# Kernel optimization log

Hardware: AMD Instinct MI355X
Metric: run time of the kernel (lower is better)

## Reference

```python
import jax, jax.numpy as jnp
import numpy as np

B, S, D, H = 256, 200, 256, 4
HD = D // H
R = 16  # HIE reduced rank (hardcoded in module)
EPS = 1e-12


def setup_inputs() -> dict:
    key = jax.random.key(0)
    ks = jax.random.split(key, 32)
    w = lambda k, sh: jax.random.normal(k, sh, jnp.float32) * 0.02
    inp = {
        'input_tensor': jax.random.normal(ks[0], (B, S, D), jnp.float32),
        'fusion_tensor': jax.random.normal(ks[1], (B, S, D), jnp.float32),
        'pos_tensor': jax.random.normal(ks[2], (B, S, D), jnp.float32),
        'attention_mask': jnp.zeros((B, 1, 1, S), jnp.float32),
        # projections (stored as (in, out); apply as x @ W + b)
        'Wv': w(ks[3], (D, D)), 'bv': w(ks[4], (D,)),
        'Wqf': w(ks[5], (D, D)), 'bqf': w(ks[6], (D,)),
        'Wkf': w(ks[7], (D, D)), 'bkf': w(ks[8], (D,)),
        'Wvf': w(ks[9], (D, D)), 'bvf': w(ks[10], (D,)),
        'Wqp': w(ks[11], (D, D)), 'bqp': w(ks[12], (D,)),
        'Wkp': w(ks[13], (D, D)), 'bkp': w(ks[14], (D,)),
        'Wvp': w(ks[15], (D, D)), 'bvp': w(ks[16], (D,)),
        # output dense + LayerNorm per branch
        'Wd': w(ks[17], (D, D)), 'bd': w(ks[18], (D,)),
        'g1': jnp.ones((D,), jnp.float32), 'b1': jnp.zeros((D,), jnp.float32),
        'Wfd': w(ks[19], (D, D)), 'bfd': w(ks[20], (D,)),
        'g2': jnp.ones((D,), jnp.float32), 'b2': jnp.zeros((D,), jnp.float32),
        'Wpd': w(ks[21], (D, D)), 'bpd': w(ks[22], (D,)),
        'g3': jnp.ones((D,), jnp.float32), 'b3': jnp.zeros((D,), jnp.float32),
        # HIE parameter (n, r)
        'Wr': jax.random.normal(ks[23], (S, R), jnp.float32),
    }
    return inp


def _heads(t):
    # (B,S,D) -> (B,H,S,HD)
    return t.reshape(B, S, H, HD).transpose(0, 2, 1, 3)


def _layernorm(x, g, b):
    m = jnp.mean(x, axis=-1, keepdims=True)
    v = jnp.mean((x - m) ** 2, axis=-1, keepdims=True)
    return (x - m) * jax.lax.rsqrt(v + EPS) * g + b


def _compute(resid, value_layer, scores, mask, Wd, bd, g, b):
    s = scores / np.sqrt(HD) + mask
    probs = jax.nn.softmax(s, axis=-1)  # (attn dropout = identity in eval)
    ctx = jnp.einsum('bhqk,bhkd->bhqd', probs, value_layer)
    ctx = ctx.transpose(0, 2, 1, 3).reshape(B, S, D)
    return _layernorm(ctx @ Wd + bd + resid, g, b)


def _hie(hX, hA, Wr):
    # reduce sequence dim, batched QR on (d, r) columns
    hr = jnp.einsum('bnd,nr->brd', hX, Wr)        # (B,R,D)
    Q, _ = jnp.linalg.qr(hr.transpose(0, 2, 1))   # (B,D,R), reduced
    pX = hX @ Q                                    # (B,S,R)
    pA = hA @ Q
    pAt = (pX * pA > 0).astype(pA.dtype) * pA      # indicator gate
    return jnp.einsum('bnr,bdr->bnd', pAt, Q)


def reference(input_tensor, fusion_tensor, pos_tensor, attention_mask,
              Wv, bv, Wqf, bqf, Wkf, bkf, Wvf, bvf, Wqp, bqp, Wkp, bkp,
              Wvp, bvp, Wd, bd, g1, b1, Wfd, bfd, g2, b2, Wpd, bpd, g3, b3, Wr):
    item_v = _heads(input_tensor @ Wv + bv)
    fq = _heads(fusion_tensor @ Wqf + bqf)
    fk = _heads(fusion_tensor @ Wkf + bkf)
    fv = _heads(fusion_tensor @ Wvf + bvf)
    pq = _heads(pos_tensor @ Wqp + bqp)
    pk = _heads(pos_tensor @ Wkp + bkp)
    pv = _heads(pos_tensor @ Wvp + bvp)

    item_scores = jnp.einsum('bhqd,bhkd->bhqk', fq, fk)
    pos_scores = jnp.einsum('bhqd,bhkd->bhqk', pq, pk)
    both_scores = item_scores + pos_scores

    h = _compute(input_tensor, item_v, both_scores, attention_mask, Wd, bd, g1, b1)
    hf = _compute(fusion_tensor, fv, item_scores, attention_mask, Wfd, bfd, g2, b2)
    hp = _compute(pos_tensor, pv, pos_scores, attention_mask, Wpd, bpd, g3, b3)

    h = h + _hie(h, hf, Wr)
    return (h, hf, hp)
```

## Files before the change

### kernel.cpp

```cpp
#include <hip/hip_runtime.h>


constexpr int B_ = 256, S_ = 200, D_ = 256, H_ = 4, R_ = 16;
constexpr int M_ = B_ * S_;
constexpr size_t BSD = (size_t)B_ * S_ * D_;

typedef __attribute__((ext_vector_type(8))) short bf16x8;
typedef __attribute__((ext_vector_type(4))) short bf16x4;
typedef __attribute__((ext_vector_type(4))) float f32x4;

#if __has_builtin(__builtin_amdgcn_mfma_f32_16x16x16bf16_1k)
#define MFMA16(A, B, C) __builtin_amdgcn_mfma_f32_16x16x16bf16_1k((A), (B), (C), 0, 0, 0)
#define HAVE_MFMA16 1
#else
#define HAVE_MFMA16 0
#endif

__device__ __forceinline__ float bf2f(unsigned short u) {
  union { unsigned int i; float f; } v; v.i = ((unsigned int)u) << 16; return v.f;
}
__device__ __forceinline__ unsigned short f2bf_rne(float f) {
  union { float f; unsigned int i; } v; v.f = f;
  unsigned int u = v.i;
  u += 0x7FFFu + ((u >> 16) & 1u);
  return (unsigned short)(u >> 16);
}
__device__ __forceinline__ void split4(const float* v, ushort4& hi, ushort4& lo) {
  unsigned short h0 = f2bf_rne(v[0]), h1 = f2bf_rne(v[1]);
  unsigned short h2 = f2bf_rne(v[2]), h3 = f2bf_rne(v[3]);
  hi.x = h0; hi.y = h1; hi.z = h2; hi.w = h3;
  lo.x = f2bf_rne(v[0] - bf2f(h0)); lo.y = f2bf_rne(v[1] - bf2f(h1));
  lo.z = f2bf_rne(v[2] - bf2f(h2)); lo.w = f2bf_rne(v[3] - bf2f(h3));
}
__device__ __forceinline__ void split8(const float* v, bf16x8& hi, bf16x8& lo) {
#pragma unroll
  for (int i = 0; i < 8; ++i) {
    unsigned short h = f2bf_rne(v[i]);
    hi[i] = (short)h;
    lo[i] = (short)f2bf_rne(v[i] - bf2f(h));
  }
}

struct GemmArgs {
  const float* X[7]; const float* bias[7]; float* Y[7];
  const float* resid[7]; const float* g[7]; const float* bvec[7];
  const unsigned short* stash;
};
struct WSplitArgs { const float* W[7]; };

__global__ __launch_bounds__(256) void split_w(WSplitArgs wa, unsigned short* stash)
{
  const int z = blockIdx.y;
  const int idx = blockIdx.x * 256 + threadIdx.x;
  const int k = idx >> 8, n = idx & 255;
  const float x = wa.W[z][idx];
  const unsigned short h = f2bf_rne(x);
  const unsigned short l = f2bf_rne(x - bf2f(h));
  const size_t o = (size_t)z * 131072 + (size_t)n * 256 + k;
  stash[o] = h;
  stash[o + 65536] = l;
}

template<bool LN>
__global__ __launch_bounds__(256, 2) void gemm_mfma(GemmArgs ga)
{
  __shared__ unsigned short lds[30720];
  unsigned short* Ah = lds;
  unsigned short* Al = Ah + 128 * 40;
  unsigned short* Bh = Al + 128 * 40;
  unsigned short* Bl = Bh + 256 * 40;
  const int t = threadIdx.x;
  const int z = blockIdx.y;
  const int m0 = blockIdx.x * 128;
  const float* __restrict__ X = ga.X[z];
  const float* __restrict__ bias = ga.bias[z];
  float* __restrict__ Y = ga.Y[z];
  const unsigned short* __restrict__ Wst = ga.stash + (size_t)z * 131072;
  const int w = t >> 6, lane = t & 63;
  const int wm = w >> 1, wn = w & 1;
  const int lrow = lane & 15;
  const int lk = (lane >> 4) << 3;
  const int rsub = (lane >> 4) << 2;

  f32x4 acc[4][8];
#pragma unroll
  for (int mf = 0; mf < 4; ++mf)
#pragma unroll
    for (int nf = 0; nf < 8; ++nf)
#pragma unroll
      for (int r = 0; r < 4; ++r) acc[mf][nf][r] = 0.f;

  for (int k0 = 0; k0 < 256; k0 += 32) {
#pragma unroll
    for (int i = 0; i < 2; ++i) {
      int c = t + i * 256;
      int r = c >> 2, c8 = (c & 3) << 3;
      float xv[8];
      *reinterpret_cast<float4*>(&xv[0]) =
          *reinterpret_cast<const float4*>(X + (size_t)(m0 + r) * 256 + k0 + c8);
      *reinterpret_cast<float4*>(&xv[4]) =
          *reinterpret_cast<const float4*>(X + (size_t)(m0 + r) * 256 + k0 + c8 + 4);
      bf16x8 hv, lv;
      split8(xv, hv, lv);
      *reinterpret_cast<bf16x8*>(&Ah[r * 40 + c8]) = hv;
      *reinterpret_cast<bf16x8*>(&Al[r * 40 + c8]) = lv;
    }
#pragma unroll
    for (int i = 0; i < 4; ++i) {
      int c = t + i * 256;
      int n = c >> 2, kc = (c & 3) << 3;
      *reinterpret_cast<uint4*>(&Bh[n * 40 + kc]) =
          *reinterpret_cast<const uint4*>(Wst + (size_t)n * 256 + k0 + kc);
      *reinterpret_cast<uint4*>(&Bl[n * 40 + kc]) =
          *reinterpret_cast<const uint4*>(Wst + 65536 + (size_t)n * 256 + k0 + kc);
    }
    __syncthreads();
    bf16x8 ah[4], al[4];
#pragma unroll
    for (int mf = 0; mf < 4; ++mf) {
      int r = wm * 64 + mf * 16 + lrow;
      ah[mf] = *reinterpret_cast<const bf16x8*>(&Ah[r * 40 + lk]);
      al[mf] = *reinterpret_cast<const bf16x8*>(&Al[r * 40 + lk]);
    }
#pragma unroll
    for (int nf = 0; nf < 8; ++nf) {
      int n = wn * 128 + nf * 16 + lrow;
      bf16x8 bh = *reinterpret_cast<const bf16x8*>(&Bh[n * 40 + lk]);
      bf16x8 bl = *reinterpret_cast<const bf16x8*>(&Bl[n * 40 + lk]);
#pragma unroll
      for (int mf = 0; mf < 4; ++mf) {
        acc[mf][nf] = __builtin_amdgcn_mfma_f32_16x16x32_bf16(ah[mf], bh, acc[mf][nf], 0, 0, 0);
        acc[mf][nf] = __builtin_amdgcn_mfma_f32_16x16x32_bf16(al[mf], bh, acc[mf][nf], 0, 0, 0);
        acc[mf][nf] = __builtin_amdgcn_mfma_f32_16x16x32_bf16(ah[mf], bl, acc[mf][nf], 0, 0, 0);
      }
    }
    __syncthreads();
  }

  if (!LN) {
#pragma unroll
    for (int nf = 0; nf < 8; ++nf) {
      const int coln = wn * 128 + nf * 16 + lrow;
      const float bb = bias[coln];
#pragma unroll
      for (int mf = 0; mf < 4; ++mf)
#pragma unroll
        for (int r = 0; r < 4; ++r) {
          const size_t row = (size_t)(m0 + wm * 64 + mf * 16 + rsub + r);
          Y[row * 256 + coln] = acc[mf][nf][r] + bb;
        }
    }
  } else {
    const float* __restrict__ resid = ga.resid[z];
    const float* __restrict__ gv = ga.g[z];
    const float* __restrict__ bv = ga.bvec[z];
    float s_[4][4], q_[4][4];
#pragma unroll
    for (int mf = 0; mf < 4; ++mf)
#pragma unroll
      for (int r = 0; r < 4; ++r) { s_[mf][r] = 0.f; q_[mf][r] = 0.f; }
#pragma unroll
    for (int nf = 0; nf < 8; ++nf) {
      const int coln = wn * 128 + nf * 16 + lrow;
      const float bb = bias[coln];
#pragma unroll
      for (int mf = 0; mf < 4; ++mf)
#pragma unroll
        for (int r = 0; r < 4; ++r) {
          const size_t row = (size_t)(m0 + wm * 64 + mf * 16 + rsub + r);
          float v = acc[mf][nf][r] + bb + resid[row * 256 + coln];
          acc[mf][nf][r] = v;
          s_[mf][r] += v;
          q_[mf][r] = fmaf(v, v, q_[mf][r]);
        }
    }
#pragma unroll
    for (int mf = 0; mf < 4; ++mf)
#pragma unroll
      for (int r = 0; r < 4; ++r) {
        float sv = s_[mf][r], qv = q_[mf][r];
        sv += __shfl_xor(sv, 1); qv += __shfl_xor(qv, 1);
        sv += __shfl_xor(sv, 2); qv += __shfl_xor(qv, 2);
        sv += __shfl_xor(sv, 4); qv += __shfl_xor(qv, 4);
        sv += __shfl_xor(sv, 8); qv += __shfl_xor(qv, 8);
        s_[mf][r] = sv; q_[mf][r] = qv;
      }
    __syncthreads();
    float* red = (float*)lds;
    if (lrow == 0) {
#pragma unroll
      for (int mf = 0; mf < 4; ++mf)
#pragma unroll
        for (int r = 0; r < 4; ++r) {
          int rl = wm * 64 + mf * 16 + rsub + r;
          red[rl * 4 + wn * 2 + 0] = s_[mf][r];
          red[rl * 4 + wn * 2 + 1] = q_[mf][r];
        }
    }
    __syncthreads();
#pragma unroll
    for (int mf = 0; mf < 4; ++mf)
#pragma unroll
      for (int r = 0; r < 4; ++r) {
        int rl = wm * 64 + mf * 16 + rsub + r;
        float st = red[rl * 4 + 0] + red[rl * 4 + 2];
        float qt = red[rl * 4 + 1] + red[rl * 4 + 3];
        float mean = st * (1.0f / 256.0f);
        float var = qt * (1.0f / 256.0f) - mean * mean;
        s_[mf][r] = mean;
        q_[mf][r] = rsqrtf(var + 1e-12f);
      }
#pragma unroll
    for (int nf = 0; nf < 8; ++nf) {
      const int coln = wn * 128 + nf * 16 + lrow;
      const float gg = gv[coln], be = bv[coln];
#pragma unroll
      for (int mf = 0; mf < 4; ++mf)
#pragma unroll
        for (int r = 0; r < 4; ++r) {
          const size_t row = (size_t)(m0 + wm * 64 + mf * 16 + rsub + r);
          Y[row * 256 + coln] = (acc[mf][nf][r] - s_[mf][r]) * q_[mf][r] * gg + be;
        }
    }
  }
}

__global__ __launch_bounds__(256) void attn_mfma(
    const float* __restrict__ Qf, const float* __restrict__ Kf,
    const float* __restrict__ Qp, const float* __restrict__ Kp,
    const float* __restrict__ Vi, const float* __restrict__ Vf,
    const float* __restrict__ Vp, const float* __restrict__ mask,
    float* __restrict__ Ch, float* __restrict__ Cf, float* __restrict__ Cp)
{
  __shared__ unsigned short su[21504];
  __shared__ float mt[32];
  constexpr int KFH = 0,     KFL = 2816,  KPH = 5632,  KPL = 8448;
  constexpr int VIH = 11264, VIL = 13824, VFH = 16384, VPH = 18944;
  const int t = threadIdx.x;
  const int mtile = blockIdx.x, h = blockIdx.y, b = blockIdx.z;
  const int w = t >> 6, lane = t & 63, lg = lane >> 4, lm = lane & 15;
  const int mbase = mtile * 128 + w * 32;
  const bool wactive = (mbase < 200);
  const size_t bh = (size_t)b * 200 * 256 + (size_t)h * 64;

  bf16x8 qfh[2][2], qfl[2][2], qph[2][2], qpl[2][2];
#pragma unroll
  for (int mf2 = 0; mf2 < 2; ++mf2) {
    int gq = mbase + mf2 * 16 + lm; if (gq > 199) gq = 199;
    const size_t qb = bh + (size_t)gq * 256;
#pragma unroll
    for (int ks = 0; ks < 2; ++ks) {
      float qv[8];
      *reinterpret_cast<float4*>(&qv[0]) =
          *reinterpret_cast<const float4*>(Qf + qb + ks * 32 + lg * 8);
      *reinterpret_cast<float4*>(&qv[4]) =
          *reinterpret_cast<const float4*>(Qf + qb + ks * 32 + lg * 8 + 4);
      split8(qv, qfh[mf2][ks], qfl[mf2][ks]);
      *reinterpret_cast<float4*>(&qv[0]) =
          *reinterpret_cast<const float4*>(Qp + qb + ks * 32 + lg * 8);
      *reinterpret_cast<float4*>(&qv[4]) =
          *reinterpret_cast<const float4*>(Qp + qb + ks * 32 + lg * 8 + 4);
      split8(qv, qph[mf2][ks], qpl[mf2][ks]);
    }
  }

  f32x4 aH[4][2], aF[4][2], aP[4][2];
#pragma unroll
  for (int df = 0; df < 4; ++df)
#pragma unroll
    for (int mf2 = 0; mf2 < 2; ++mf2)
#pragma unroll
      for (int r = 0; r < 4; ++r) { aH[df][mf2][r] = 0.f; aF[df][mf2][r] = 0.f; aP[df][mf2][r] = 0.f; }
  float lH[2] = {0.f, 0.f}, lF[2] = {0.f, 0.f}, lP[2] = {0.f, 0.f};

  for (int kt = 0; kt < 200; kt += 32) {
#pragma unroll
    for (int i = 0; i < 2; ++i) {
      int idx = t + i * 256;
      const int pk = idx >> 8;
      const int rr = (idx >> 3) & 31;
      const int c8 = (idx & 7) << 3;
      int grow = kt + rr; if (grow > 199) grow = 199;
      const float* src = pk ? Kp : Kf;
      float kv8[8];
      *reinterpret_cast<float4*>(&kv8[0]) =
          *reinterpret_cast<const float4*>(src + bh + (size_t)grow * 256 + c8);
      *reinterpret_cast<float4*>(&kv8[4]) =
          *reinterpret_cast<const float4*>(src + bh + (size_t)grow * 256 + c8 + 4);
      bf16x8 hv, lv;
      split8(kv8, hv, lv);
      const int KH = pk ? KPH : KFH;
      const int KL = pk ? KPL : KFL;
      *reinterpret_cast<bf16x8*>(&su[KH + rr * 88 + c8]) = hv;
      *reinterpret_cast<bf16x8*>(&su[KL + rr * 88 + c8]) = lv;
    }
#pragma unroll
    for (int i = 0; i < 2; ++i) {
      int idx = t + i * 256;
      int d = idx & 63, kv4i = (idx >> 6) << 2;
      float vv[4];
      ushort4 hv, lv;
      size_t rb[4];
#pragma unroll
      for (int j = 0; j < 4; ++j) {
        int grow = kt + kv4i + j; if (grow > 199) grow = 199;
        rb[j] = bh + (size_t)grow * 256 + d;
      }
#pragma unroll
      for (int j = 0; j < 4; ++j) vv[j] = Vi[rb[j]];
      split4(vv, hv, lv);
      *reinterpret_cast<ushort4*>(&su[VIH + d * 40 + kv4i]) = hv;
      *reinterpret_cast<ushort4*>(&su[VIL + d * 40 + kv4i]) = lv;
      hv.x = f2bf_rne(Vf[rb[0]]); hv.y = f2bf_rne(Vf[rb[1]]);
      hv.z = f2bf_rne(Vf[rb[2]]); hv.w = f2bf_rne(Vf[rb[3]]);
      *reinterpret_cast<ushort4*>(&su[VFH + d * 40 + kv4i]) = hv;
      hv.x = f2bf_rne(Vp[rb[0]]); hv.y = f2bf_rne(Vp[rb[1]]);
      hv.z = f2bf_rne(Vp[rb[2]]); hv.w = f2bf_rne(Vp[rb[3]]);
      *reinterpret_cast<ushort4*>(&su[VPH + d * 40 + kv4i]) = hv;
    }
    if (t < 32) mt[t] = (kt + t < 200) ? mask[(size_t)b * 200 + kt + t] : -1e30f;
    __syncthreads();

    if (wactive) {
      f32x4 si[2][2], sp[2][2];
#pragma unroll
      for (int kvf = 0; kvf < 2; ++kvf)
#pragma unroll
        for (int mf2 = 0; mf2 < 2; ++mf2)
#pragma unroll
          for (int r = 0; r < 4; ++r) { si[kvf][mf2][r] = 0.f; sp[kvf][mf2][r] = 0.f; }
#pragma unroll
      for (int ks = 0; ks < 2; ++ks)
#pragma unroll
        for (int kvf = 0; kvf < 2; ++kvf) {
          bf16x8 kh = *reinterpret_cast<const bf16x8*>(&su[KFH + (kvf * 16 + lm) * 88 + ks * 32 + lg * 8]);
          bf16x8 kl = *reinterpret_cast<const bf16x8*>(&su[KFL + (kvf * 16 + lm) * 88 + ks * 32 + lg * 8]);
#pragma unroll
          for (int mf2 = 0; mf2 < 2; ++mf2) {
            si[kvf][mf2] = __builtin_amdgcn_mfma_f32_16x16x32_bf16(kh, qfh[mf2][ks], si[kvf][mf2], 0, 0, 0);
            si[kvf][mf2] = __builtin_amdgcn_mfma_f32_16x16x32_bf16(kl, qfh[mf2][ks], si[kvf][mf2], 0, 0, 0);
            si[kvf][mf2] = __builtin_amdgcn_mfma_f32_16x16x32_bf16(kh, qfl[mf2][ks], si[kvf][mf2], 0, 0, 0);
          }
          kh = *reinterpret_cast<const bf16x8*>(&su[KPH + (kvf * 16 + lm) * 88 + ks * 32 + lg * 8]);
          kl = *reinterpret_cast<const bf16x8*>(&su[KPL + (kvf * 16 + lm) * 88 + ks * 32 + lg * 8]);
#pragma unroll
          for (int mf2 = 0; mf2 < 2; ++mf2) {
            sp[kvf][mf2] = __builtin_amdgcn_mfma_f32_16x16x32_bf16(kh, qph[mf2][ks], sp[kvf][mf2], 0, 0, 0);
            sp[kvf][mf2] = __builtin_amdgcn_mfma_f32_16x16x32_bf16(kl, qph[mf2][ks], sp[kvf][mf2], 0, 0, 0);
            sp[kvf][mf2] = __builtin_amdgcn_mfma_f32_16x16x32_bf16(kh, qpl[mf2][ks], sp[kvf][mf2], 0, 0, 0);
          }
        }

      f32x4 ph[2][2], pf[2][2], pp[2][2];
      float4 mv[2];
      mv[0] = *reinterpret_cast<const float4*>(&mt[lg * 4]);
      mv[1] = *reinterpret_cast<const float4*>(&mt[16 + lg * 4]);
#pragma unroll
      for (int kvf = 0; kvf < 2; ++kvf)
#pragma unroll
        for (int mf2 = 0; mf2 < 2; ++mf2)
#pragma unroll
          for (int r = 0; r < 4; ++r) {
            float mj = (r == 0) ? mv[kvf].x : (r == 1) ? mv[kvf].y : (r == 2) ? mv[kvf].z : mv[kvf].w;
            float ai = fmaf(si[kvf][mf2][r], 0.125f, mj);
            float ap = sp[kvf][mf2][r] * 0.125f;
            float vF = __expf(ai);
            float vP = __expf(ap + mj);
            float vH = __expf(ai + ap);
            pf[kvf][mf2][r] = vF; pp[kvf][mf2][r] = vP; ph[kvf][mf2][r] = vH;
            lF[mf2] += vF; lP[mf2] += vP; lH[mf2] += vH;
          }

#if HAVE_MFMA16
#pragma unroll
      for (int kvf = 0; kvf < 2; ++kvf) {
        bf16x4 bH[2], bL[2], bF[2], bP[2];
#pragma unroll
        for (int mf2 = 0; mf2 < 2; ++mf2) {
#pragma unroll
          for (int i = 0; i < 4; ++i) {
            float vH = ph[kvf][mf2][i];
            unsigned short hh = f2bf_rne(vH);
            bH[mf2][i] = (short)hh;
            bL[mf2][i] = (short)f2bf_rne(vH - bf2f(hh));
            bF[mf2][i] = (short)f2bf_rne(pf[kvf][mf2][i]);
            bP[mf2][i] = (short)f2bf_rne(pp[kvf][mf2][i]);
          }
        }
#pragma unroll
        for (int df = 0; df < 4; ++df) {
          const int rowb = (df * 16 + lm) * 40 + kvf * 16 + lg * 4;
          bf16x4 vih = *reinterpret_cast<const bf16x4*>(&su[VIH + rowb]);
          bf16x4 vil = *reinterpret_cast<const bf16x4*>(&su[VIL + rowb]);
          bf16x4 vfh = *reinterpret_cast<const bf16x4*>(&su[VFH + rowb]);
          bf16x4 vph = *reinterpret_cast<const bf16x4*>(&su[VPH + rowb]);
#pragma unroll
          for (int mf2 = 0; mf2 < 2; ++mf2) {
            aH[df][mf2] = MFMA16(vih, bH[mf2], aH[df][mf2]);
            aH[df][mf2] = MFMA16(vil, bH[mf2], aH[df][mf2]);
            aH[df][mf2] = MFMA16(vih, bL[mf2], aH[df][mf2]);
            aF[df][mf2] = MFMA16(vfh, bF[mf2], aF[df][mf2]);
            aP[df][mf2] = MFMA16(vph, bP[mf2], aP[df][mf2]);
          }
        }
      }
#else
#define PV3(P, VH, VL, ACC)                                                    \
      {                                                                        \
        bf16x8 Bh[2], Bl[2];                                                   \
        _Pragma("unroll")                                                      \
        for (int mf2 = 0; mf2 < 2; ++mf2) {                                    \
          _Pragma("unroll")                                                    \
          for (int i = 0; i < 8; ++i) {                                        \
            int src = ((((lg & 1) * 2 + (i >> 2)) << 4) | lm);                 \
            float t0 = __shfl(P[0][mf2][i & 3], src);                          \
            float t1 = __shfl(P[1][mf2][i & 3], src);                          \
            float v = (lg < 2) ? t0 : t1;                                      \
            unsigned short hh = f2bf_rne(v);                                   \
            Bh[mf2][i] = (short)hh;                                            \
            Bl[mf2][i] = (short)f2bf_rne(v - bf2f(hh));                        \
          }                                                                    \
        }                                                                      \
        _Pragma("unroll")                                                      \
        for (int df = 0; df < 4; ++df) {                                       \
          bf16x8 vh = *reinterpret_cast<const bf16x8*>(&su[VH + (df * 16 + lm) * 40 + lg * 8]); \
          bf16x8 vl = *reinterpret_cast<const bf16x8*>(&su[VL + (df * 16 + lm) * 40 + lg * 8]); \
          _Pragma("unroll")                                                    \
          for (int mf2 = 0; mf2 < 2; ++mf2) {                                  \
            ACC[df][mf2] = __builtin_amdgcn_mfma_f32_16x16x32_bf16(vh, Bh[mf2], ACC[df][mf2], 0, 0, 0); \
            ACC[df][mf2] = __builtin_amdgcn_mfma_f32_16x16x32_bf16(vl, Bh[mf2], ACC[df][mf2], 0, 0, 0); \
            ACC[df][mf2] = __builtin_amdgcn_mfma_f32_16x16x32_bf16(vh, Bl[mf2], ACC[df][mf2], 0, 0, 0); \
          }                                                                    \
        }                                                                      \
      }
#define PV1(P, VH, ACC)                                                        \
      {                                                                        \
        bf16x8 Bh[2];                                                          \
        _Pragma("unroll")                                                      \
        for (int mf2 = 0; mf2 < 2; ++mf2) {                                    \
          _Pragma("unroll")                                                    \
          for (int i = 0; i < 8; ++i) {                                        \
            int src = ((((lg & 1) * 2 + (i >> 2)) << 4) | lm);                 \
            float t0 = __shfl(P[0][mf2][i & 3], src);                          \
            float t1 = __shfl(P[1][mf2][i & 3], src);                          \
            float v = (lg < 2) ? t0 : t1;                                      \
            Bh[mf2][i] = (short)f2bf_rne(v);                                   \
          }                                                                    \
        }                                                                      \
        _Pragma("unroll")                                                      \
        for (int df = 0; df < 4; ++df) {                                       \
          bf16x8 vh = *reinterpret_cast<const bf16x8*>(&su[VH + (df * 16 + lm) * 40 + lg * 8]); \
          _Pragma("unroll")                                                    \
          for (int mf2 = 0; mf2 < 2; ++mf2)                                    \
            ACC[df][mf2] = __builtin_amdgcn_mfma_f32_16x16x32_bf16(vh, Bh[mf2], ACC[df][mf2], 0, 0, 0); \
        }                                                                      \
      }
      PV3(ph, VIH, VIL, aH)
      PV1(pf, VFH, aF)
      PV1(pp, VPH, aP)
#undef PV3
#undef PV1
#endif
    }
    __syncthreads();
  }

#pragma unroll
  for (int mf2 = 0; mf2 < 2; ++mf2) {
    lH[mf2] += __shfl_xor(lH[mf2], 16); lH[mf2] += __shfl_xor(lH[mf2], 32);
    lF[mf2] += __shfl_xor(lF[mf2], 16); lF[mf2] += __shfl_xor(lF[mf2], 32);
    lP[mf2] += __shfl_xor(lP[mf2], 16); lP[mf2] += __shfl_xor(lP[mf2], 32);
  }

#pragma unroll
  for (int mf2 = 0; mf2 < 2; ++mf2) {
    int gq = mbase + mf2 * 16 + lm;
    if (gq < 200) {
      const size_t base = bh + (size_t)gq * 256;
      const float iH = 1.f / lH[mf2], iF = 1.f / lF[mf2], iP = 1.f / lP[mf2];
#pragma unroll
      for (int df = 0; df < 4; ++df) {
        float4 o;
        o.x = aH[df][mf2][0] * iH; o.y = aH[df][mf2][1] * iH;
        o.z = aH[df][mf2][2] * iH; o.w = aH[df][mf2][3] * iH;
        *reinterpret_cast<float4*>(Ch + base + df * 16 + lg * 4) = o;
        o.x = aF[df][mf2][0] * iF; o.y = aF[df][mf2][1] * iF;
        o.z = aF[df][mf2][2] * iF; o.w = aF[df][mf2][3] * iF;
        *reinterpret_cast<float4*>(Cf + base + df * 16 + lg * 4) = o;
        o.x = aP[df][mf2][0] * iP; o.y = aP[df][mf2][1] * iP;
        o.z = aP[df][mf2][2] * iP; o.w = aP[df][mf2][3] * iP;
        *reinterpret_cast<float4*>(Cp + base + df * 16 + lg * 4) = o;
      }
    }
  }
}

__global__ __launch_bounds__(256) void hie_hr_kernel(
    const float* __restrict__ h, const float* __restrict__ Wr, float* __restrict__ hr)
{
  __shared__ float wrs[3200];
  const int b = blockIdx.x, t = threadIdx.x;
  for (int i = t; i < 3200; i += 256) wrs[i] = Wr[i];
  __syncthreads();
  double acc[16];
#pragma unroll
  for (int r = 0; r < 16; ++r) acc[r] = 0.0;
  const float* hb = h + (size_t)b * 200 * 256;
  for (int n = 0; n < 200; ++n) {
    float hv = hb[(size_t)n * 256 + t];
#pragma unroll
    for (int r = 0; r < 16; ++r) acc[r] += (double)(hv * wrs[n * 16 + r]);
  }
#pragma unroll
  for (int r = 0; r < 16; ++r) hr[((size_t)b * 16 + r) * 256 + t] = (float)acc[r];
}

__global__ __launch_bounds__(256) void hie_qr_kernel(
    const float* __restrict__ hr, float* __restrict__ Qg)
{
  __shared__ float Qs[16][256];
  __shared__ double red[4];
  const int b = blockIdx.x, t = threadIdx.x;
  const int wid = t >> 6, lane = t & 63;
  const float* A = hr + (size_t)b * 4096;
#pragma unroll 1
  for (int j = 0; j < 16; ++j) {
    double v = (double)A[j * 256 + t];
#pragma unroll 1
    for (int i = 0; i < j; ++i) {
      float qi = Qs[i][t];
      double p = (double)qi * v;
#pragma unroll
      for (int off = 32; off; off >>= 1) p += __shfl_xor(p, off);
      if (lane == 0) red[wid] = p;
      __syncthreads();
      double dot = red[0] + red[1] + red[2] + red[3];
      __syncthreads();
      v -= dot * (double)qi;
    }
    double nn = v * v;
#pragma unroll
    for (int off = 32; off; off >>= 1) nn += __shfl_xor(nn, off);
    if (lane == 0) red[wid] = nn;
    __syncthreads();
    double nrm = sqrt(red[0] + red[1] + red[2] + red[3]);
    __syncthreads();
    float qv = (float)(v / nrm);
    Qs[j][t] = qv;
    Qg[(size_t)b * 4096 + j * 256 + t] = qv;
    __syncthreads();
  }
}

__global__ __launch_bounds__(256) void hie_pxgate(
    const float* __restrict__ hX, const float* __restrict__ hA,
    const float* __restrict__ Qg, float* __restrict__ patp)
{
  __shared__ float Qs[16][260];
  __shared__ float ha[16][260];
  __shared__ float hbx[16][260];
  const int ch = blockIdx.x, b = blockIdx.y, t = threadIdx.x;
  const int chunk = ch * 16;
  for (int i = t; i < 4096; i += 256) Qs[i >> 8][i & 255] = Qg[(size_t)b * 4096 + i];
#pragma unroll
  for (int i = 0; i < 4; ++i) {
    int c = t + i * 256;
    int rr = c >> 6, c4 = (c & 63) << 2;
    int n = chunk + rr;
    if (n < 200) {
      *reinterpret_cast<float4*>(&ha[rr][c4]) =
          *reinterpret_cast<const float4*>(hX + ((size_t)b * 200 + n) * 256 + c4);
      *reinterpret_cast<float4*>(&hbx[rr][c4]) =
          *reinterpret_cast<const float4*>(hA + ((size_t)b * 200 + n) * 256 + c4);
    }
  }
  __syncthreads();
  const int nl = t >> 4, r = t & 15;
  int n = chunk + nl;
  if (n < 200) {
    double ax = 0.0, aa = 0.0;
#pragma unroll
    for (int d4 = 0; d4 < 256; d4 += 4) {
      float4 qv = *reinterpret_cast<const float4*>(&Qs[r][d4]);
      float4 hv = *reinterpret_cast<const float4*>(&ha[nl][d4]);
      ax += (double)(hv.x * qv.x + hv.y * qv.y + hv.z * qv.z + hv.w * qv.w);
      hv = *reinterpret_cast<const float4*>(&hbx[nl][d4]);
      aa += (double)(hv.x * qv.x + hv.y * qv.y + hv.z * qv.z + hv.w * qv.w);
    }
    float px = (float)ax, pa = (float)aa;
    patp[((size_t)b * 200 + n) * 16 + r] = (px * pa > 0.0f) ? pa : 0.0f;
  }
}

__global__ __launch_bounds__(256) void hie_final_kernel(
    const float* __restrict__ h, const float* __restrict__ pat,
    const float* __restrict__ Qg, float* __restrict__ outp)
{
  __shared__ float Qs[16][260];
  __shared__ float pt[16][16];
  const int ch = blockIdx.x, b = blockIdx.y, t = threadIdx.x;
  const int chunk = ch * 16;
  for (int i = t; i < 4096; i += 256) Qs[i >> 8][i & 255] = Qg[(size_t)b * 4096 + i];
  const int nl = t >> 4, r = t & 15;
  {
    int n = chunk + nl;
    pt[nl][r] = (n < 200) ? pat[((size_t)b * 200 + n) * 16 + r] : 0.0f;
  }
  __syncthreads();
#pragma unroll 1
  for (int j = 0; j < 16; ++j) {
    int n = chunk + j;
    if (n >= 200) break;
    float acc = h[((size_t)b * 200 + n) * 256 + t];
#pragma unroll
    for (int rr = 0; rr < 16; ++rr) acc = fmaf(pt[j][rr], Qs[rr][t], acc);
    outp[((size_t)b * 200 + n) * 256 + t] = acc;
  }
}

__global__ void diag_kernel(float* out, float val, int n) {
  int i = blockIdx.x * 256 + threadIdx.x;
  if (i < n) out[i] = (i == 0) ? val : 0.0f;
}

extern "C" void kernel_launch(void* const* d_in, const int* in_sizes, int n_in,
                              void* d_out, int out_size, void* d_ws, size_t ws_size,
                              hipStream_t stream)
{
  (void)in_sizes; (void)n_in;
  const float* input  = (const float*)d_in[0];
  const float* fusion = (const float*)d_in[1];
  const float* pos    = (const float*)d_in[2];
  const float* mask   = (const float*)d_in[3];
  const float* Wv  = (const float*)d_in[4];  const float* bv  = (const float*)d_in[5];
  const float* Wqf = (const float*)d_in[6];  const float* bqf = (const float*)d_in[7];
  const float* Wkf = (const float*)d_in[8];  const float* bkf = (const float*)d_in[9];
  const float* Wvf = (const float*)d_in[10]; const float* bvf = (const float*)d_in[11];
  const float* Wqp = (const float*)d_in[12]; const float* bqp = (const float*)d_in[13];
  const float* Wkp = (const float*)d_in[14]; const float* bkp = (const float*)d_in[15];
  const float* Wvp = (const float*)d_in[16]; const float* bvp = (const float*)d_in[17];
  const float* Wd  = (const float*)d_in[18]; const float* bd  = (const float*)d_in[19];
  const float* g1  = (const float*)d_in[20]; const float* b1  = (const float*)d_in[21];
  const float* Wfd = (const float*)d_in[22]; const float* bfd = (const float*)d_in[23];
  const float* g2  = (const float*)d_in[24]; const float* b2  = (const float*)d_in[25];
  const float* Wpd = (const float*)d_in[26]; const float* bpd = (const float*)d_in[27];
  const float* g3  = (const float*)d_in[28]; const float* b3  = (const float*)d_in[29];
  const float* Wr  = (const float*)d_in[30];

  const size_t required = 7 * BSD * 4;
  if (ws_size < required) {
    diag_kernel<<<(out_size + 255) / 256, 256, 0, stream>>>(
        (float*)d_out, (float)(ws_size >> 20), out_size);
    return;
  }

  float* W0 = (float*)d_ws;
  float* O0 = (float*)d_out;
  float* O1 = O0 + BSD;
  float* O2 = O0 + 2 * BSD;
  float* s_fq = W0;
  float* s_fk = W0 + BSD;
  float* s_pq = W0 + 2 * BSD;
  float* s_pk = W0 + 3 * BSD;
  float* s_iv = W0 + 4 * BSD;
  float* s_fv = W0 + 5 * BSD;
  float* s_pv = W0 + 6 * BSD;
  float* hrb  = W0;
  float* Qb   = W0 + 1048576;
  float* patb = W0 + 2097152;
  unsigned short* stash1 = (unsigned short*)d_out;
  unsigned short* stash2 = (unsigned short*)(W0 + 4 * 1048576);

  dim3 Blk(256);

  WSplitArgs w7;
  w7.W[0] = Wqf; w7.W[1] = Wkf; w7.W[2] = Wqp; w7.W[3] = Wkp;
  w7.W[4] = Wv;  w7.W[5] = Wvf; w7.W[6] = Wvp;
  split_w<<<dim3(256, 7), Blk, 0, stream>>>(w7, stash1);

  GemmArgs pa = {};
  pa.X[0] = fusion; pa.bias[0] = bqf; pa.Y[0] = s_fq;
  pa.X[1] = fusion; pa.bias[1] = bkf; pa.Y[1] = s_fk;
  pa.X[2] = pos;    pa.bias[2] = bqp; pa.Y[2] = s_pq;
  pa.X[3] = pos;    pa.bias[3] = bkp; pa.Y[3] = s_pk;
  pa.X[4] = input;  pa.bias[4] = bv;  pa.Y[4] = s_iv;
  pa.X[5] = fusion; pa.bias[5] = bvf; pa.Y[5] = s_fv;
  pa.X[6] = pos;    pa.bias[6] = bvp; pa.Y[6] = s_pv;
  pa.stash = stash1;
  gemm_mfma<false><<<dim3(M_ / 128, 7), Blk, 0, stream>>>(pa);

  attn_mfma<<<dim3(2, H_, B_), Blk, 0, stream>>>(s_fq, s_fk, s_pq, s_pk,
                                                 s_iv, s_fv, s_pv, mask, O0, O1, O2);

  WSplitArgs w3;
  w3.W[0] = Wd; w3.W[1] = Wfd; w3.W[2] = Wpd;
  split_w<<<dim3(256, 3), Blk, 0, stream>>>(w3, stash2);

  GemmArgs da = {};
  da.X[0] = O0; da.bias[0] = bd;  da.Y[0] = O0; da.resid[0] = input;  da.g[0] = g1; da.bvec[0] = b1;
  da.X[1] = O1; da.bias[1] = bfd; da.Y[1] = O1; da.resid[1] = fusion; da.g[1] = g2; da.bvec[1] = b2;
  da.X[2] = O2; da.bias[2] = bpd; da.Y[2] = O2; da.resid[2] = pos;    da.g[2] = g3; da.bvec[2] = b3;
  da.stash = stash2;
  gemm_mfma<true><<<dim3(M_ / 128, 3), Blk, 0, stream>>>(da);

  hie_hr_kernel<<<B_, Blk, 0, stream>>>(O0, Wr, hrb);
  hie_qr_kernel<<<B_, Blk, 0, stream>>>(hrb, Qb);
  hie_pxgate<<<dim3(13, B_), Blk, 0, stream>>>(O0, O1, Qb, patb);
  hie_final_kernel<<<dim3(13, B_), Blk, 0, stream>>>(O0, patb, Qb, O0);
}
```

Baseline: 753.5 us.

## Emit pre-split bf16 hi/lo pairs from projection GEMM and factor softmax exponentials

The projection GEMM epilogue now writes each output as a packed bf16 hi/lo pair in one 32-bit word. The attention kernel reads these pairs and unpacks them with bit operations instead of redoing the float-to-bf16 split on every Q/K/V load. The combined-score exponential is now computed as exp(F)*exp(P)*exp(-mask), which drops one transcendental per score element. The factored product can overflow or lose precision if the per-branch scores are large, since there is no max-subtraction.

```diff
diff --git a/kernel.cpp b/kernel.cpp
--- a/kernel.cpp
+++ b/kernel.cpp
@@ -25,13 +25,6 @@
   u += 0x7FFFu + ((u >> 16) & 1u);
   return (unsigned short)(u >> 16);
 }
-__device__ __forceinline__ void split4(const float* v, ushort4& hi, ushort4& lo) {
-  unsigned short h0 = f2bf_rne(v[0]), h1 = f2bf_rne(v[1]);
-  unsigned short h2 = f2bf_rne(v[2]), h3 = f2bf_rne(v[3]);
-  hi.x = h0; hi.y = h1; hi.z = h2; hi.w = h3;
-  lo.x = f2bf_rne(v[0] - bf2f(h0)); lo.y = f2bf_rne(v[1] - bf2f(h1));
-  lo.z = f2bf_rne(v[2] - bf2f(h2)); lo.w = f2bf_rne(v[3] - bf2f(h3));
-}
 __device__ __forceinline__ void split8(const float* v, bf16x8& hi, bf16x8& lo) {
 #pragma unroll
   for (int i = 0; i < 8; ++i) {
@@ -39,6 +32,18 @@
     hi[i] = (short)h;
     lo[i] = (short)f2bf_rne(v[i] - bf2f(h));
   }
+}
+__device__ __forceinline__ void unpack8(uint4 a, uint4 b, bf16x8& hi, bf16x8& lo) {
+  union { bf16x8 v; unsigned int u[4]; } H, L;
+  H.u[0] = (a.x & 0xffffu) | (a.y << 16);
+  H.u[1] = (a.z & 0xffffu) | (a.w << 16);
+  H.u[2] = (b.x & 0xffffu) | (b.y << 16);
+  H.u[3] = (b.z & 0xffffu) | (b.w << 16);
+  L.u[0] = (a.x >> 16) | (a.y & 0xffff0000u);
+  L.u[1] = (a.z >> 16) | (a.w & 0xffff0000u);
+  L.u[2] = (b.x >> 16) | (b.y & 0xffff0000u);
+  L.u[3] = (b.z >> 16) | (b.w & 0xffff0000u);
+  hi = H.v; lo = L.v;
 }
 
 struct GemmArgs {
@@ -61,7 +66,7 @@
   stash[o + 65536] = l;
 }
 
-template<bool LN>
+template<int MODE>
 __global__ __launch_bounds__(256, 2) void gemm_mfma(GemmArgs ga)
 {
   __shared__ unsigned short lds[30720];
@@ -137,7 +142,8 @@
     __syncthreads();
   }
 
-  if (!LN) {
+  if (MODE == 0) {
+    unsigned int* Yu = (unsigned int*)Y;
 #pragma unroll
     for (int nf = 0; nf < 8; ++nf) {
       const int coln = wn * 128 + nf * 16 + lrow;
@@ -147,7 +153,10 @@
 #pragma unroll
         for (int r = 0; r < 4; ++r) {
           const size_t row = (size_t)(m0 + wm * 64 + mf * 16 + rsub + r);
-          Y[row * 256 + coln] = acc[mf][nf][r] + bb;
+          float v = acc[mf][nf][r] + bb;
+          unsigned short hh = f2bf_rne(v);
+          unsigned short ll = f2bf_rne(v - bf2f(hh));
+          Yu[row * 256 + coln] = (unsigned int)hh | ((unsigned int)ll << 16);
         }
     }
   } else {
@@ -226,14 +235,15 @@
 }
 
 __global__ __launch_bounds__(256) void attn_mfma(
-    const float* __restrict__ Qf, const float* __restrict__ Kf,
-    const float* __restrict__ Qp, const float* __restrict__ Kp,
-    const float* __restrict__ Vi, const float* __restrict__ Vf,
-    const float* __restrict__ Vp, const float* __restrict__ mask,
+    const unsigned int* __restrict__ Qf, const unsigned int* __restrict__ Kf,
+    const unsigned int* __restrict__ Qp, const unsigned int* __restrict__ Kp,
+    const unsigned int* __restrict__ Vi, const unsigned int* __restrict__ Vf,
+    const unsigned int* __restrict__ Vp, const float* __restrict__ mask,
     float* __restrict__ Ch, float* __restrict__ Cf, float* __restrict__ Cp)
 {
   __shared__ unsigned short su[21504];
   __shared__ float mt[32];
+  __shared__ float emt[32];
   constexpr int KFH = 0,     KFL = 2816,  KPH = 5632,  KPL = 8448;
   constexpr int VIH = 11264, VIL = 13824, VFH = 16384, VPH = 18944;
   const int t = threadIdx.x;
@@ -250,17 +260,13 @@
     const size_t qb = bh + (size_t)gq * 256;
 #pragma unroll
     for (int ks = 0; ks < 2; ++ks) {
-      float qv[8];
-      *reinterpret_cast<float4*>(&qv[0]) =
-          *reinterpret_cast<const float4*>(Qf + qb + ks * 32 + lg * 8);
-      *reinterpret_cast<float4*>(&qv[4]) =
-          *reinterpret_cast<const float4*>(Qf + qb + ks * 32 + lg * 8 + 4);
-      split8(qv, qfh[mf2][ks], qfl[mf2][ks]);
-      *reinterpret_cast<float4*>(&qv[0]) =
-          *reinterpret_cast<const float4*>(Qp + qb + ks * 32 + lg * 8);
-      *reinterpret_cast<float4*>(&qv[4]) =
-          *reinterpret_cast<const float4*>(Qp + qb + ks * 32 + lg * 8 + 4);
-      split8(qv, qph[mf2][ks], qpl[mf2][ks]);
+      const size_t o = qb + ks * 32 + lg * 8;
+      uint4 a = *reinterpret_cast<const uint4*>(Qf + o);
+      uint4 bb = *reinterpret_cast<const uint4*>(Qf + o + 4);
+      unpack8(a, bb, qfh[mf2][ks], qfl[mf2][ks]);
+      a = *reinterpret_cast<const uint4*>(Qp + o);
+      bb = *reinterpret_cast<const uint4*>(Qp + o + 4);
+      unpack8(a, bb, qph[mf2][ks], qpl[mf2][ks]);
     }
   }
 
@@ -281,14 +287,12 @@
       const int rr = (idx >> 3) & 31;
       const int c8 = (idx & 7) << 3;
       int grow = kt + rr; if (grow > 199) grow = 199;
-      const float* src = pk ? Kp : Kf;
-      float kv8[8];
-      *reinterpret_cast<float4*>(&kv8[0]) =
-          *reinterpret_cast<const float4*>(src + bh + (size_t)grow * 256 + c8);
-      *reinterpret_cast<float4*>(&kv8[4]) =
-          *reinterpret_cast<const float4*>(src + bh + (size_t)grow * 256 + c8 + 4);
+      const unsigned int* src = pk ? Kp : Kf;
+      const size_t o = bh + (size_t)grow * 256 + c8;
+      uint4 a = *reinterpret_cast<const uint4*>(src + o);
+      uint4 bb = *reinterpret_cast<const uint4*>(src + o + 4);
       bf16x8 hv, lv;
-      split8(kv8, hv, lv);
+      unpack8(a, bb, hv, lv);
       const int KH = pk ? KPH : KFH;
       const int KL = pk ? KPL : KFL;
       *reinterpret_cast<bf16x8*>(&su[KH + rr * 88 + c8]) = hv;
@@ -298,27 +302,35 @@
     for (int i = 0; i < 2; ++i) {
       int idx = t + i * 256;
       int d = idx & 63, kv4i = (idx >> 6) << 2;
-      float vv[4];
-      ushort4 hv, lv;
       size_t rb[4];
 #pragma unroll
       for (int j = 0; j < 4; ++j) {
         int grow = kt + kv4i + j; if (grow > 199) grow = 199;
         rb[j] = bh + (size_t)grow * 256 + d;
       }
-#pragma unroll
-      for (int j = 0; j < 4; ++j) vv[j] = Vi[rb[j]];
-      split4(vv, hv, lv);
+      unsigned int u0 = Vi[rb[0]], u1 = Vi[rb[1]], u2 = Vi[rb[2]], u3 = Vi[rb[3]];
+      ushort4 hv, lv;
+      hv.x = (unsigned short)u0; hv.y = (unsigned short)u1;
+      hv.z = (unsigned short)u2; hv.w = (unsigned short)u3;
+      lv.x = (unsigned short)(u0 >> 16); lv.y = (unsigned short)(u1 >> 16);
+      lv.z = (unsigned short)(u2 >> 16); lv.w = (unsigned short)(u3 >> 16);
       *reinterpret_cast<ushort4*>(&su[VIH + d * 40 + kv4i]) = hv;
       *reinterpret_cast<ushort4*>(&su[VIL + d * 40 + kv4i]) = lv;
-      hv.x = f2bf_rne(Vf[rb[0]]); hv.y = f2bf_rne(Vf[rb[1]]);
-      hv.z = f2bf_rne(Vf[rb[2]]); hv.w = f2bf_rne(Vf[rb[3]]);
+      u0 = Vf[rb[0]]; u1 = Vf[rb[1]]; u2 = Vf[rb[2]]; u3 = Vf[rb[3]];
+      hv.x = (unsigned short)u0; hv.y = (unsigned short)u1;
+      hv.z = (unsigned short)u2; hv.w = (unsigned short)u3;
       *reinterpret_cast<ushort4*>(&su[VFH + d * 40 + kv4i]) = hv;
-      hv.x = f2bf_rne(Vp[rb[0]]); hv.y = f2bf_rne(Vp[rb[1]]);
-      hv.z = f2bf_rne(Vp[rb[2]]); hv.w = f2bf_rne(Vp[rb[3]]);
+      u0 = Vp[rb[0]]; u1 = Vp[rb[1]]; u2 = Vp[rb[2]]; u3 = Vp[rb[3]];
+      hv.x = (unsigned short)u0; hv.y = (unsigned short)u1;
+      hv.z = (unsigned short)u2; hv.w = (unsigned short)u3;
       *reinterpret_cast<ushort4*>(&su[VPH + d * 40 + kv4i]) = hv;
     }
-    if (t < 32) mt[t] = (kt + t < 200) ? mask[(size_t)b * 200 + kt + t] : -1e30f;
+    if (t < 32) {
+      const bool valid = (kt + t < 200);
+      const float mj = valid ? mask[(size_t)b * 200 + kt + t] : -1e30f;
+      mt[t] = mj;
+      emt[t] = valid ? __expf(-mj) : 0.f;
+    }
     __syncthreads();
 
     if (wactive) {
@@ -352,9 +364,11 @@
         }
 
       f32x4 ph[2][2], pf[2][2], pp[2][2];
-      float4 mv[2];
+      float4 mv[2], ev[2];
       mv[0] = *reinterpret_cast<const float4*>(&mt[lg * 4]);
       mv[1] = *reinterpret_cast<const float4*>(&mt[16 + lg * 4]);
+      ev[0] = *reinterpret_cast<const float4*>(&emt[lg * 4]);
+      ev[1] = *reinterpret_cast<const float4*>(&emt[16 + lg * 4]);
 #pragma unroll
       for (int kvf = 0; kvf < 2; ++kvf)
 #pragma unroll
@@ -362,11 +376,10 @@
 #pragma unroll
           for (int r = 0; r < 4; ++r) {
             float mj = (r == 0) ? mv[kvf].x : (r == 1) ? mv[kvf].y : (r == 2) ? mv[kvf].z : mv[kvf].w;
-            float ai = fmaf(si[kvf][mf2][r], 0.125f, mj);
-            float ap = sp[kvf][mf2][r] * 0.125f;
-            float vF = __expf(ai);
-            float vP = __expf(ap + mj);
-            float vH = __expf(ai + ap);
+            float ej = (r == 0) ? ev[kvf].x : (r == 1) ? ev[kvf].y : (r == 2) ? ev[kvf].z : ev[kvf].w;
+            float vF = __expf(fmaf(si[kvf][mf2][r], 0.125f, mj));
+            float vP = __expf(fmaf(sp[kvf][mf2][r], 0.125f, mj));
+            float vH = vF * vP * ej;
             pf[kvf][mf2][r] = vF; pp[kvf][mf2][r] = vP; ph[kvf][mf2][r] = vH;
             lF[mf2] += vF; lP[mf2] += vP; lH[mf2] += vH;
           }
@@ -687,10 +700,13 @@
   pa.X[5] = fusion; pa.bias[5] = bvf; pa.Y[5] = s_fv;
   pa.X[6] = pos;    pa.bias[6] = bvp; pa.Y[6] = s_pv;
   pa.stash = stash1;
-  gemm_mfma<false><<<dim3(M_ / 128, 7), Blk, 0, stream>>>(pa);
-
-  attn_mfma<<<dim3(2, H_, B_), Blk, 0, stream>>>(s_fq, s_fk, s_pq, s_pk,
-                                                 s_iv, s_fv, s_pv, mask, O0, O1, O2);
+  gemm_mfma<0><<<dim3(M_ / 128, 7), Blk, 0, stream>>>(pa);
+
+  attn_mfma<<<dim3(2, H_, B_), Blk, 0, stream>>>(
+      (const unsigned int*)s_fq, (const unsigned int*)s_fk,
+      (const unsigned int*)s_pq, (const unsigned int*)s_pk,
+      (const unsigned int*)s_iv, (const unsigned int*)s_fv,
+      (const unsigned int*)s_pv, mask, O0, O1, O2);
 
   WSplitArgs w3;
   w3.W[0] = Wd; w3.W[1] = Wfd; w3.W[2] = Wpd;
@@ -701,7 +717,7 @@
   da.X[1] = O1; da.bias[1] = bfd; da.Y[1] = O1; da.resid[1] = fusion; da.g[1] = g2; da.bvec[1] = b2;
   da.X[2] = O2; da.bias[2] = bpd; da.Y[2] = O2; da.resid[2] = pos;    da.g[2] = g3; da.bvec[2] = b3;
   da.stash = stash2;
-  gemm_mfma<true><<<dim3(M_ / 128, 3), Blk, 0, stream>>>(da);
+  gemm_mfma<1><<<dim3(M_ / 128, 3), Blk, 0, stream>>>(da);
 
   hie_hr_kernel<<<B_, Blk, 0, stream>>>(O0, Wr, hrb);
   hie_qr_kernel<<<B_, Blk, 0, stream>>>(hrb, Qb);
```

Result: no change. 738.8 us (-2.0%).
